# Performance work log

Hardware: AMD Instinct MI355X
Metric: run time of the kernel (lower is better)

## Reference

```python
import jax, jax.numpy as jnp
import numpy as np

B, N2, N3, D = 16, 1024, 2048, 128


def setup_inputs() -> dict:
    key = jax.random.key(0)
    k1, k2 = jax.random.split(key)
    desc2d = jax.random.normal(k1, (B * N2, D), dtype=jnp.float32)
    desc3d = jax.random.normal(k2, (B * N3, D), dtype=jnp.float32)
    # uniform, sorted batch ids (equal-size segments -> jit-friendly ragged layout)
    idx2d = jnp.repeat(jnp.arange(B, dtype=jnp.int64), N2)
    idx3d = jnp.repeat(jnp.arange(B, dtype=jnp.int64), N3)
    return {"desc2d": desc2d, "idx2d": idx2d, "desc3d": desc3d, "idx3d": idx3d}


def reference(desc2d, idx2d, desc3d, idx3d):
    # number of batches from sorted batch ids (static, computed on host)
    nb = int(np.asarray(idx2d)[-1]) + 1
    n2 = desc2d.shape[0] // nb
    n3 = desc3d.shape[0] // nb
    d2 = desc2d.reshape(nb, n2, -1)  # [B, n2, D]
    d3 = desc3d.reshape(nb, n3, -1)  # [B, n3, D]
    d2 = d2 / jnp.linalg.norm(d2, axis=-1, keepdims=True)
    d3 = d3 / jnp.linalg.norm(d3, axis=-1, keepdims=True)
    sim = jnp.einsum('bid,bjd->bij', d3, d2)  # cosine similarity [B, n3, n2]
    # zero-pad one extra row and column per batch (dustbin), as in the original
    return jnp.pad(sim, ((0, 0), (0, 1), (0, 1)))
```

## Files before the change

kernel.cpp:

```cpp
#include <hip/hip_runtime.h>
#include <hip/hip_bf16.h>

#define NB   16
#define N2   1024
#define N3   2048
#define DD   128
#define OROWS (N3 + 1)
#define OCOLS (N2 + 1)

typedef __attribute__((ext_vector_type(8))) __bf16 bf16x8;
typedef __attribute__((ext_vector_type(4))) float  f32x4;

static __device__ __forceinline__ unsigned pack_bf16x2(float a, float b) {
    unsigned ua = __float_as_uint(a);
    ua = (ua + 0x7FFF + ((ua >> 16) & 1)) >> 16;
    unsigned ub = __float_as_uint(b);
    ub = (ub + 0x7FFF + ((ub >> 16) & 1)) & 0xFFFF0000u;
    return ua | ub;
}

__global__ void normalize_d2(const float* __restrict__ d2,
                             unsigned short* __restrict__ ws) {
    const int row = blockIdx.x * 8 + (threadIdx.x >> 5);
    const int l   = threadIdx.x & 31;
    const float4 v = *reinterpret_cast<const float4*>(d2 + (size_t)row * DD + l * 4);
    float ss = v.x * v.x + v.y * v.y + v.z * v.z + v.w * v.w;
    #pragma unroll
    for (int off = 16; off; off >>= 1) ss += __shfl_xor(ss, off);
    const float s = rsqrtf(ss);
    ushort4 o;
    o.x = (unsigned short)(pack_bf16x2(v.x * s, v.y * s) & 0xFFFF);
    o.y = (unsigned short)(pack_bf16x2(v.y * s, 0.f) & 0xFFFF);
    unsigned w0 = pack_bf16x2(v.x * s, v.y * s);
    unsigned w1 = pack_bf16x2(v.z * s, v.w * s);
    uint2 w; w.x = w0; w.y = w1;
    *reinterpret_cast<uint2*>(ws + (size_t)row * DD + l * 4) = w;
}

__global__ __launch_bounds__(512, 1)
void gemm_kernel(const float* __restrict__ d3,
                 const unsigned short* __restrict__ d2n,
                 float* __restrict__ out) {
    __shared__ __align__(16) char smem[49152];

    const int hw  = blockIdx.x;
    const int blk = (hw & 7) * 32 + (hw >> 3);
    const int b   = blk >> 4;
    const int ti  = blk & 15;
    const int t   = threadIdx.x;

    const float* gA = d3 + (size_t)(b * N3 + ti * 128) * DD;
    const char*  gB = (const char*)d2n + ((size_t)(b * N2) << 8);

    auto stage = [&](int c) {
        const char* src = gB + (size_t)c * 16384;
        char* dst = smem + 16384 * ((c + 2) % 3);
        #pragma unroll
        for (int it = 0; it < 2; ++it) {
            int o    = it * 8192 + t * 16;
            int row  = o >> 8;
            int scol = (o & 255) ^ ((row & 7) << 4);
            __builtin_amdgcn_global_load_lds(
                (const __attribute__((address_space(1))) void*)(src + row * 256 + scol),
                (__attribute__((address_space(3))) void*)(dst + o), 16, 0, 0);
        }
    };

    const int arow  = t >> 2;
    const int apart = t & 3;
    float4 av[8];
    #pragma unroll
    for (int i = 0; i < 8; ++i)
        av[i] = *reinterpret_cast<const float4*>(gA + (size_t)arow * DD + apart * 32 + i * 4);
    stage(0);

    {
        float ss = 0.f;
        #pragma unroll
        for (int i = 0; i < 8; ++i)
            ss += av[i].x * av[i].x + av[i].y * av[i].y + av[i].z * av[i].z + av[i].w * av[i].w;
        ss += __shfl_xor(ss, 1);
        ss += __shfl_xor(ss, 2);
        const float s = rsqrtf(ss);
        const int aswz = (arow & 7) << 4;
        #pragma unroll
        for (int j = 0; j < 4; ++j) {
            uint4 w;
            w.x = pack_bf16x2(av[2 * j].x * s,     av[2 * j].y * s);
            w.y = pack_bf16x2(av[2 * j].z * s,     av[2 * j].w * s);
            w.z = pack_bf16x2(av[2 * j + 1].x * s, av[2 * j + 1].y * s);
            w.w = pack_bf16x2(av[2 * j + 1].z * s, av[2 * j + 1].w * s);
            int colb = apart * 64 + j * 16;
            *reinterpret_cast<uint4*>(smem + arow * 256 + (colb ^ aswz)) = w;
        }
    }
    asm volatile("s_waitcnt vmcnt(0) lgkmcnt(0)" ::: "memory");
    __builtin_amdgcn_s_barrier();
    __builtin_amdgcn_sched_barrier(0);

    const int wid = t >> 6;
    const int l   = t & 63;
    const int wm  = (wid >> 2) * 64;
    const int wn  = (wid & 3) * 16;
    const int lr  = l & 15;
    const int kq  = l >> 4;
    const int sw  = (lr & 7) << 4;

    bf16x8 af[4][4];
    #pragma unroll
    for (int ks = 0; ks < 4; ++ks) {
        const int kb = ks * 64 + kq * 16;
        #pragma unroll
        for (int mi = 0; mi < 4; ++mi) {
            int r = wm + mi * 16 + lr;
            af[ks][mi] = *reinterpret_cast<const bf16x8*>(smem + r * 256 + (kb ^ sw));
        }
    }
    asm volatile("s_waitcnt lgkmcnt(0)" ::: "memory");
    __builtin_amdgcn_s_barrier();
    __builtin_amdgcn_sched_barrier(0);

    float* obase = out + (size_t)b * OROWS * OCOLS + (size_t)(ti * 128) * OCOLS;

    for (int nj = 0; nj < 16; ++nj) {
        const char* bbuf = smem + 16384 * ((nj + 2) % 3);

        f32x4 acc[4] = {};
        #pragma unroll
        for (int ks = 0; ks < 4; ++ks) {
            const int kb = ks * 64 + kq * 16;
            bf16x8 bfr = *reinterpret_cast<const bf16x8*>(bbuf + (wn + lr) * 256 + (kb ^ sw));
            #pragma unroll
            for (int mi = 0; mi < 4; ++mi)
                acc[mi] = __builtin_amdgcn_mfma_f32_16x16x32_bf16(
                    af[ks][mi], bfr, acc[mi], 0, 0, 0);
        }

        if (nj == 0) { stage(1); stage(2); }
        else if (nj + 2 < 16) stage(nj + 2);

        #pragma unroll
        for (int mi = 0; mi < 4; ++mi) {
            #pragma unroll
            for (int i = 0; i < 4; ++i) {
                int r = wm + mi * 16 + kq * 4 + i;
                int c = nj * 64 + wn + lr;
                obase[(size_t)r * OCOLS + c] = acc[mi][i];
            }
        }

        if (nj < 14) {
            asm volatile("s_waitcnt vmcnt(18)" ::: "memory");
            __builtin_amdgcn_s_barrier();
            __builtin_amdgcn_sched_barrier(0);
        } else if (nj == 14) {
            asm volatile("s_waitcnt vmcnt(16)" ::: "memory");
            __builtin_amdgcn_s_barrier();
            __builtin_amdgcn_sched_barrier(0);
        }
    }

    if (t < 128)
        obase[(size_t)t * OCOLS + N2] = 0.0f;
    if (ti == 15) {
        float* last = out + (size_t)b * OROWS * OCOLS + (size_t)N3 * OCOLS;
        for (int c = t; c < OCOLS; c += 512) last[c] = 0.0f;
    }
}

extern "C" void kernel_launch(void* const* d_in, const int* in_sizes, int n_in,
                              void* d_out, int out_size, void* d_ws, size_t ws_size,
                              hipStream_t stream) {
    (void)in_sizes; (void)n_in; (void)out_size; (void)ws_size;
    const float* desc2d = (const float*)d_in[0];
    const float* desc3d = (const float*)d_in[2];

    unsigned short* d2n = (unsigned short*)d_ws;
    float* out = (float*)d_out;

    normalize_d2<<<(NB * N2) / 8, 256, 0, stream>>>(desc2d, d2n);
    gemm_kernel<<<NB * (N3 / 128), 512, 0, stream>>>(desc3d, d2n, out);
}
```

Baseline: 39.77 us.

## Halve GEMM row tile to 64 and run two 256-thread blocks per CU

```diff
diff --git a/kernel.cpp b/kernel.cpp
--- a/kernel.cpp
+++ b/kernel.cpp
@@ -28,36 +28,35 @@
     #pragma unroll
     for (int off = 16; off; off >>= 1) ss += __shfl_xor(ss, off);
     const float s = rsqrtf(ss);
-    ushort4 o;
-    o.x = (unsigned short)(pack_bf16x2(v.x * s, v.y * s) & 0xFFFF);
-    o.y = (unsigned short)(pack_bf16x2(v.y * s, 0.f) & 0xFFFF);
-    unsigned w0 = pack_bf16x2(v.x * s, v.y * s);
-    unsigned w1 = pack_bf16x2(v.z * s, v.w * s);
-    uint2 w; w.x = w0; w.y = w1;
+    uint2 w;
+    w.x = pack_bf16x2(v.x * s, v.y * s);
+    w.y = pack_bf16x2(v.z * s, v.w * s);
     *reinterpret_cast<uint2*>(ws + (size_t)row * DD + l * 4) = w;
 }
 
-__global__ __launch_bounds__(512, 1)
+__global__ __launch_bounds__(256, 2)
 void gemm_kernel(const float* __restrict__ d3,
                  const unsigned short* __restrict__ d2n,
                  float* __restrict__ out) {
-    __shared__ __align__(16) char smem[49152];
+    __shared__ __align__(16) char smem[65536];
 
     const int hw  = blockIdx.x;
-    const int blk = (hw & 7) * 32 + (hw >> 3);
-    const int b   = blk >> 4;
-    const int ti  = blk & 15;
+    const int blk = (hw & 7) * 64 + (hw >> 3);
+    const int b   = blk >> 5;
+    const int ti  = blk & 31;
     const int t   = threadIdx.x;
 
-    const float* gA = d3 + (size_t)(b * N3 + ti * 128) * DD;
+    const float* gA = d3 + (size_t)(b * N3 + ti * 64) * DD;
     const char*  gB = (const char*)d2n + ((size_t)(b * N2) << 8);
+
+    char* const aLds = smem + 49152;
 
     auto stage = [&](int c) {
         const char* src = gB + (size_t)c * 16384;
         char* dst = smem + 16384 * ((c + 2) % 3);
         #pragma unroll
-        for (int it = 0; it < 2; ++it) {
-            int o    = it * 8192 + t * 16;
+        for (int it = 0; it < 4; ++it) {
+            int o    = it * 4096 + t * 16;
             int row  = o >> 8;
             int scol = (o & 255) ^ ((row & 7) << 4);
             __builtin_amdgcn_global_load_lds(
@@ -91,7 +90,7 @@
             w.z = pack_bf16x2(av[2 * j + 1].x * s, av[2 * j + 1].y * s);
             w.w = pack_bf16x2(av[2 * j + 1].z * s, av[2 * j + 1].w * s);
             int colb = apart * 64 + j * 16;
-            *reinterpret_cast<uint4*>(smem + arow * 256 + (colb ^ aswz)) = w;
+            *reinterpret_cast<uint4*>(aLds + arow * 256 + (colb ^ aswz)) = w;
         }
     }
     asm volatile("s_waitcnt vmcnt(0) lgkmcnt(0)" ::: "memory");
@@ -100,27 +99,19 @@
 
     const int wid = t >> 6;
     const int l   = t & 63;
-    const int wm  = (wid >> 2) * 64;
-    const int wn  = (wid & 3) * 16;
+    const int wm  = wid * 16;
     const int lr  = l & 15;
     const int kq  = l >> 4;
     const int sw  = (lr & 7) << 4;
 
-    bf16x8 af[4][4];
+    bf16x8 af[4];
     #pragma unroll
     for (int ks = 0; ks < 4; ++ks) {
         const int kb = ks * 64 + kq * 16;
-        #pragma unroll
-        for (int mi = 0; mi < 4; ++mi) {
-            int r = wm + mi * 16 + lr;
-            af[ks][mi] = *reinterpret_cast<const bf16x8*>(smem + r * 256 + (kb ^ sw));
-        }
+        af[ks] = *reinterpret_cast<const bf16x8*>(aLds + (wm + lr) * 256 + (kb ^ sw));
     }
-    asm volatile("s_waitcnt lgkmcnt(0)" ::: "memory");
-    __builtin_amdgcn_s_barrier();
-    __builtin_amdgcn_sched_barrier(0);
 
-    float* obase = out + (size_t)b * OROWS * OCOLS + (size_t)(ti * 128) * OCOLS;
+    float* obase = out + (size_t)b * OROWS * OCOLS + (size_t)(ti * 64) * OCOLS;
 
     for (int nj = 0; nj < 16; ++nj) {
         const char* bbuf = smem + 16384 * ((nj + 2) % 3);
@@ -129,28 +120,30 @@
         #pragma unroll
         for (int ks = 0; ks < 4; ++ks) {
             const int kb = ks * 64 + kq * 16;
-            bf16x8 bfr = *reinterpret_cast<const bf16x8*>(bbuf + (wn + lr) * 256 + (kb ^ sw));
             #pragma unroll
-            for (int mi = 0; mi < 4; ++mi)
-                acc[mi] = __builtin_amdgcn_mfma_f32_16x16x32_bf16(
-                    af[ks][mi], bfr, acc[mi], 0, 0, 0);
+            for (int ni = 0; ni < 4; ++ni) {
+                bf16x8 bfr = *reinterpret_cast<const bf16x8*>(
+                    bbuf + (ni * 16 + lr) * 256 + (kb ^ sw));
+                acc[ni] = __builtin_amdgcn_mfma_f32_16x16x32_bf16(
+                    af[ks], bfr, acc[ni], 0, 0, 0);
+            }
         }
 
         if (nj == 0) { stage(1); stage(2); }
         else if (nj + 2 < 16) stage(nj + 2);
 
         #pragma unroll
-        for (int mi = 0; mi < 4; ++mi) {
+        for (int i = 0; i < 4; ++i) {
+            int r = wm + kq * 4 + i;
             #pragma unroll
-            for (int i = 0; i < 4; ++i) {
-                int r = wm + mi * 16 + kq * 4 + i;
-                int c = nj * 64 + wn + lr;
-                obase[(size_t)r * OCOLS + c] = acc[mi][i];
+            for (int ni = 0; ni < 4; ++ni) {
+                int c = nj * 64 + ni * 16 + lr;
+                obase[(size_t)r * OCOLS + c] = acc[ni][i];
             }
         }
 
         if (nj < 14) {
-            asm volatile("s_waitcnt vmcnt(18)" ::: "memory");
+            asm volatile("s_waitcnt vmcnt(20)" ::: "memory");
             __builtin_amdgcn_s_barrier();
             __builtin_amdgcn_sched_barrier(0);
         } else if (nj == 14) {
@@ -160,11 +153,11 @@
         }
     }
 
-    if (t < 128)
+    if (t < 64)
         obase[(size_t)t * OCOLS + N2] = 0.0f;
-    if (ti == 15) {
+    if (ti == 31) {
         float* last = out + (size_t)b * OROWS * OCOLS + (size_t)N3 * OCOLS;
-        for (int c = t; c < OCOLS; c += 512) last[c] = 0.0f;
+        for (int c = t; c < OCOLS; c += 256) last[c] = 0.0f;
     }
 }
 
@@ -179,5 +172,5 @@
     float* out = (float*)d_out;
 
     normalize_d2<<<(NB * N2) / 8, 256, 0, stream>>>(desc2d, d2n);
-    gemm_kernel<<<NB * (N3 / 128), 512, 0, stream>>>(desc3d, d2n, out);
+    gemm_kernel<<<NB * (N3 / 64), 256, 0, stream>>>(desc3d, d2n, out);
 }
```

Measured after the change: 40.39 us. About the same (+1.5%).
